# Performance work log

Hardware: AMD Instinct MI355X
Metric: run time of the kernel (lower is better)

Reference implementation:

```python
import jax, jax.numpy as jnp
import numpy as np

B, L, D_IN, D_OUT, K = 2, 4096, 256, 256, 16


def setup_inputs() -> dict:
    key = jax.random.key(0)
    k_u, k_ev, k_ew, k_m = jax.random.split(key, 4)
    u = jax.random.normal(k_u, (B, L, D_IN), dtype=jnp.float32)
    eigenvectors = jax.random.normal(k_ev, (K, L), dtype=jnp.float32)
    # original takes loaded eigenvalues ** 0.25; emulate positive spectrum then 0.25 power
    eigenvalues = jax.random.uniform(k_ew, (K,), dtype=jnp.float32, minval=1e-3, maxval=1.0) ** 0.25
    # xavier_uniform_ for M of shape (k, d_in, d_out): bound = sqrt(6/(d_in+d_out))
    bound = float(np.sqrt(6.0 / (D_IN + D_OUT)))
    M = jax.random.uniform(k_m, (K, D_IN, D_OUT), dtype=jnp.float32, minval=-bound, maxval=bound)
    return {"u": u, "eigenvectors": eigenvectors, "eigenvalues": eigenvalues, "M": M}


def reference(u, eigenvectors, eigenvalues, M):
    # u: (B, L, D); eigenvectors: (k, L); eigenvalues: (k,); M: (k, D_in, D_out)
    Lseq = u.shape[1]
    ev_fft = jnp.fft.rfft(eigenvectors, axis=-1)          # (k, F) complex
    u_fft = jnp.fft.rfft(jnp.swapaxes(u, 1, 2), axis=-1)  # (B, D, F)
    p_fft = u_fft[:, None, :, :] * ev_fft[None, :, None, :]  # (B, k, D, F)
    conv = jnp.fft.irfft(p_fft, n=Lseq, axis=-1)          # (B, k, D, L)
    return jnp.einsum('bkdl,k,kdp->blp', conv, eigenvalues, M)
```

## Files before the change

### kernel.cpp

```cpp
#include <hip/hip_runtime.h>


typedef unsigned int uint;
using u16x8 = __attribute__((ext_vector_type(8))) unsigned short;
using s16x8 = __attribute__((ext_vector_type(8))) short;
using f32x4 = __attribute__((ext_vector_type(4))) float;

__device__ __forceinline__ unsigned short f2bf(float f) {
  uint u = __float_as_uint(f);
  uint r = (u + 0x7FFF + ((u >> 16) & 1)) >> 16;
  return (unsigned short)r;
}
__device__ __forceinline__ float bf2f(unsigned short h) {
  return __uint_as_float(((uint)h) << 16);
}

template <int NT>
__device__ __forceinline__ void fft4096(float2* __restrict__ a,
                                        float2* __restrict__ b,
                                        const float2* __restrict__ tw, int tid) {
  float2* src = a;
  float2* dst = b;
#pragma unroll
  for (int s = 0; s < 12; s += 2) {
    const int m = 1 << s;
#pragma unroll
    for (int it = 0; it < 1024 / NT; ++it) {
      int idx = tid + it * NT;
      int i   = idx & (m - 1);
      int jm  = idx - i;
      float2 A0 = src[idx];
      float2 B0 = src[idx + 1024];
      float2 C0 = src[idx + 2048];
      float2 D0 = src[idx + 3072];
      float2 w1 = tw[jm];
      float2 w2 = make_float2(w1.x * w1.x - w1.y * w1.y, 2.f * w1.x * w1.y);
      float2 w3 = make_float2(w2.x * w1.x - w2.y * w1.y, w2.x * w1.y + w2.y * w1.x);
      float acx = A0.x + C0.x, acy = A0.y + C0.y;
      float amx = A0.x - C0.x, amy = A0.y - C0.y;
      float bdx = B0.x + D0.x, bdy = B0.y + D0.y;
      float bmx = B0.x - D0.x, bmy = B0.y - D0.y;
      float2 y0 = make_float2(acx + bdx, acy + bdy);
      float2 t2 = make_float2(acx - bdx, acy - bdy);
      float2 t1 = make_float2(amx + bmy, amy - bmx);
      float2 t3 = make_float2(amx - bmy, amy + bmx);
      int base = idx + 3 * jm;
      dst[base]         = y0;
      dst[base + m]     = make_float2(w1.x * t1.x - w1.y * t1.y, w1.x * t1.y + w1.y * t1.x);
      dst[base + 2 * m] = make_float2(w2.x * t2.x - w2.y * t2.y, w2.x * t2.y + w2.y * t2.x);
      dst[base + 3 * m] = make_float2(w3.x * t3.x - w3.y * t3.y, w3.x * t3.y + w3.y * t3.x);
    }
    __syncthreads();
    float2* t = src; src = dst; dst = t;
  }
}

template <int NT>
__device__ __forceinline__ void build_tw(float2* tw, int tid) {
  for (int t = tid; t < 1024; t += NT) {
    float ang = -(float)t * (6.283185307179586f / 4096.0f);
    float s, c;
    sincosf(ang, &s, &c);
    tw[t] = make_float2(c, s);
  }
}

__global__ __launch_bounds__(256) void tr_M(const float* __restrict__ M,
                                            unsigned short* __restrict__ Mt) {
  __shared__ float t[64][65];
  const int k = blockIdx.z, d0 = blockIdx.x * 64, p0 = blockIdx.y * 64;
  const int r = threadIdx.x >> 2, c0 = (threadIdx.x & 3) * 16;
  const float* src = M + ((size_t)k * 256 + d0) * 256 + p0;
#pragma unroll
  for (int j = 0; j < 4; ++j) {
    float4 v = *(const float4*)(src + (size_t)r * 256 + c0 + j * 4);
    t[r][c0 + j * 4 + 0] = v.x;
    t[r][c0 + j * 4 + 1] = v.y;
    t[r][c0 + j * 4 + 2] = v.z;
    t[r][c0 + j * 4 + 3] = v.w;
  }
  __syncthreads();
  u16x8 o0, o1;
#pragma unroll
  for (int j = 0; j < 8; ++j) o0[j] = f2bf(t[c0 + j][r]);
#pragma unroll
  for (int j = 0; j < 8; ++j) o1[j] = f2bf(t[c0 + 8 + j][r]);
  unsigned short* dst = Mt + ((size_t)k * 256 + p0 + r) * 256 + d0 + c0;
  *(u16x8*)dst = o0;
  *(u16x8*)(dst + 8) = o1;
}

__global__ __launch_bounds__(1024) void fft_fwd(const float* __restrict__ u,
                                                const float* __restrict__ ev,
                                                const float* __restrict__ lam,
                                                unsigned short* __restrict__ Ut,
                                                float* __restrict__ Hbuf) {
  __shared__ float2 A[4096];
  __shared__ float2 Bb[4096];
  __shared__ float2 tw[1024];
  const int tid = threadIdx.x;
  const int bid = blockIdx.x;
  build_tw<1024>(tw, tid);

  if (bid < 256) {
    const int plane = bid >> 7, pair = bid & 127;
    const int d0 = pair * 2;
    const float* ub = u + (size_t)plane * 4096 * 256 + d0;
#pragma unroll
    for (int i = 0; i < 4; ++i) {
      int l = tid + i * 1024;
      A[l] = *(const float2*)(ub + (size_t)l * 256);
    }
    __syncthreads();
    fft4096<1024>(A, Bb, tw, tid);
    unsigned short* Up = Ut + (size_t)plane * 4096 * 256 + d0;
#pragma unroll
    for (int i = 0; i < 2; ++i) {
      int f = tid + i * 1024;
      float u0x, u0y, u1x, u1y;
      if (f == 0) {
        float2 X0 = A[0], Xn = A[2048];
        u0x = X0.x; u1x = X0.y;
        u0y = Xn.x; u1y = Xn.y;
      } else {
        float2 Xa = A[f], Xb = A[4096 - f];
        u0x = 0.5f * (Xa.x + Xb.x);
        u0y = 0.5f * (Xa.y - Xb.y);
        u1x = 0.5f * (Xa.y + Xb.y);
        u1y = 0.5f * (Xb.x - Xa.x);
      }
      ushort2 re = make_ushort2(f2bf(u0x), f2bf(u1x));
      ushort2 im = make_ushort2(f2bf(u0y), f2bf(u1y));
      *(ushort2*)(Up + (size_t)f * 256)          = re;
      *(ushort2*)(Up + (size_t)(2048 + f) * 256) = im;
    }
  } else {
    const int k = bid - 256;
    const float* eb = ev + (size_t)k * 4096;
#pragma unroll
    for (int i = 0; i < 4; ++i) {
      int l = tid + i * 1024;
      A[l] = make_float2(eb[l], 0.0f);
    }
    __syncthreads();
    fft4096<1024>(A, Bb, tw, tid);
    const float sc = lam[k] * (1.0f / 4096.0f);
    float* Hp = Hbuf + (size_t)k * 4096;
#pragma unroll
    for (int i = 0; i < 2; ++i) {
      int f = tid + i * 1024;
      float2 X = A[f];
      Hp[f] = sc * X.x;
      Hp[2048 + f] = (f == 0) ? sc * A[2048].x : sc * X.y;
    }
  }
}

__global__ __launch_bounds__(256) void gemm_spec(const unsigned short* __restrict__ Ut,
                                                 const unsigned short* __restrict__ Mt,
                                                 const float* __restrict__ Hbuf,
                                                 float* __restrict__ Chat) {
  __shared__ unsigned short Us[128 * 256];
  __shared__ unsigned short Ms[64 * 256];
  const int p0    = blockIdx.x * 64;
  const int fb    = blockIdx.y * 64;
  const int plane = blockIdx.z;
  const int tid  = threadIdx.x;
  const int lane = tid & 63;
  const int wave = tid >> 6;

  const unsigned short* Up = Ut + (size_t)plane * 4096 * 256;
#pragma unroll
  for (int it = 0; it < 16; ++it) {
    int cl = tid + it * 256;
    int r = cl >> 5, c = cl & 31;
    int f2 = (r < 64) ? (fb + r) : (2048 + fb + (r - 64));
    u16x8 v = *(const u16x8*)(Up + (size_t)f2 * 256 + c * 8);
    *(u16x8*)(&Us[r * 256 + ((c ^ (r & 7)) * 8)]) = v;
  }

  u16x8 mreg[8];
#pragma unroll
  for (int it = 0; it < 8; ++it) {
    int cl = tid + it * 256;
    int r = cl >> 5, c = cl & 31;
    mreg[it] = *(const u16x8*)(Mt + (size_t)(p0 + r) * 256 + c * 8);
  }

  f32x4 cre[4], cim[4];
#pragma unroll
  for (int m = 0; m < 4; ++m) {
    cre[m] = (f32x4){0.f, 0.f, 0.f, 0.f};
    cim[m] = (f32x4){0.f, 0.f, 0.f, 0.f};
  }

  const int bin = fb + wave * 16 + (lane & 15);
  const int rb_re = wave * 16 + (lane & 15);
  const int rb_im = 64 + rb_re;

  for (int k = 0; k < 16; ++k) {
    if (k > 0) __syncthreads();
#pragma unroll
    for (int it = 0; it < 8; ++it) {
      int cl = tid + it * 256;
      int r = cl >> 5, c = cl & 31;
      *(u16x8*)(&Ms[r * 256 + ((c ^ (r & 7)) * 8)]) = mreg[it];
    }
    if (k < 15) {
      const unsigned short* Mk = Mt + (size_t)(k + 1) * 65536;
#pragma unroll
      for (int it = 0; it < 8; ++it) {
        int cl = tid + it * 256;
        int r = cl >> 5, c = cl & 31;
        mreg[it] = *(const u16x8*)(Mk + (size_t)(p0 + r) * 256 + c * 8);
      }
    }
    __syncthreads();

    f32x4 are[4], aim[4];
#pragma unroll
    for (int m = 0; m < 4; ++m) {
      are[m] = (f32x4){0.f, 0.f, 0.f, 0.f};
      aim[m] = (f32x4){0.f, 0.f, 0.f, 0.f};
    }
#pragma unroll
    for (int kk = 0; kk < 8; ++kk) {
      const int kc = kk * 4 + (lane >> 4);
      s16x8 bre = *(const s16x8*)(&Us[rb_re * 256 + ((kc ^ (rb_re & 7)) * 8)]);
      s16x8 bim = *(const s16x8*)(&Us[rb_im * 256 + ((kc ^ (rb_im & 7)) * 8)]);
#pragma unroll
      for (int m = 0; m < 4; ++m) {
        int row = m * 16 + (lane & 15);
        s16x8 af = *(const s16x8*)(&Ms[row * 256 + ((kc ^ (row & 7)) * 8)]);
        are[m] = __builtin_amdgcn_mfma_f32_16x16x32_bf16(af, bre, are[m], 0, 0, 0);
        aim[m] = __builtin_amdgcn_mfma_f32_16x16x32_bf16(af, bim, aim[m], 0, 0, 0);
      }
    }
    float hre = Hbuf[(size_t)k * 4096 + bin];
    float hs  = Hbuf[(size_t)k * 4096 + 2048 + bin];
    bool sp = (bin == 0);
    float him = sp ? 0.0f : hs;
    float hA  = sp ? hs : hre;
#pragma unroll
    for (int m = 0; m < 4; ++m)
#pragma unroll
      for (int i = 0; i < 4; ++i) {
        cre[m][i] += hre * are[m][i] - him * aim[m][i];
        cim[m][i] += hA * aim[m][i] + him * are[m][i];
      }
  }

  float* Cp = Chat + ((size_t)plane * 256 + p0) * 4096;
#pragma unroll
  for (int m = 0; m < 4; ++m)
#pragma unroll
    for (int i = 0; i < 4; ++i) {
      int pl = m * 16 + (lane >> 4) * 4 + i;
      Cp[(size_t)pl * 4096 + bin]        = cre[m][i];
      Cp[(size_t)pl * 4096 + 2048 + bin] = cim[m][i];
    }
}

__global__ __launch_bounds__(1024) void ifft_store(const float* __restrict__ Chat,
                                                   float* __restrict__ out) {
  __shared__ float2 A[4096];
  __shared__ float2 Bb[4096];
  __shared__ float2 tw[1024];
  const int tid = threadIdx.x;
  const int p0 = blockIdx.x * 2;
  const int plane = blockIdx.y;
  const float* C0 = Chat + ((size_t)plane * 256 + p0) * 4096;
  const float* C1 = C0 + 4096;
  build_tw<1024>(tw, tid);

  if (tid == 0) {
    A[0]    = make_float2(C0[0], -C1[0]);
    A[2048] = make_float2(C0[2048], -C1[2048]);
  } else {
    int f = tid;
    float cr0 = C0[f], ci0 = C0[2048 + f];
    float cr1 = C1[f], ci1 = C1[2048 + f];
    A[f]        = make_float2(cr0 - ci1, -(ci0 + cr1));
    A[4096 - f] = make_float2(cr0 + ci1, ci0 - cr1);
  }
  {
    int f = tid + 1024;
    float cr0 = C0[f], ci0 = C0[2048 + f];
    float cr1 = C1[f], ci1 = C1[2048 + f];
    A[f]        = make_float2(cr0 - ci1, -(ci0 + cr1));
    A[4096 - f] = make_float2(cr0 + ci1, ci0 - cr1);
  }
  __syncthreads();
  fft4096<1024>(A, Bb, tw, tid);

  float* ob = out + (size_t)plane * 4096 * 256 + p0;
#pragma unroll
  for (int i = 0; i < 4; ++i) {
    int l = tid + i * 1024;
    float2 g = A[l];
    *(float2*)(ob + (size_t)l * 256) = make_float2(g.x, -g.y);
  }
}

extern "C" void kernel_launch(void* const* d_in, const int* in_sizes, int n_in,
                              void* d_out, int out_size, void* d_ws,
                              size_t ws_size, hipStream_t stream) {
  const float* u   = (const float*)d_in[0];
  const float* ev  = (const float*)d_in[1];
  const float* lam = (const float*)d_in[2];
  const float* M   = (const float*)d_in[3];
  float* out = (float*)d_out;

  char* ws = (char*)d_ws;
  float* Hbuf        = (float*)ws;
  unsigned short* Mt = (unsigned short*)(ws + (256 << 10));
  unsigned short* Ut = (unsigned short*)(ws + (256 << 10) + (2 << 20));
  float* Chat        = (float*)(ws + (256 << 10) + (6 << 20));

  tr_M<<<dim3(4, 4, 16), 256, 0, stream>>>(M, Mt);
  fft_fwd<<<272, 1024, 0, stream>>>(u, ev, lam, Ut, Hbuf);
  gemm_spec<<<dim3(4, 32, 2), 256, 0, stream>>>(Ut, Mt, Hbuf, Chat);
  ifft_store<<<dim3(128, 2), 1024, 0, stream>>>(Chat, out);
}
```

Measured before the change: 138.4 us.

## Add transpose kernels for coalesced FFT I/O and split-K GEMM with XCD mapping

Adds separate transpose kernels so the forward FFT reads contiguous bf16 rows and the inverse FFT writes contiguous rows, replacing strided column gathers and scatters with coalesced accesses. The spectral GEMM now runs 512 threads, with two halves each covering 8 of the 16 eigen-components, then sums the halves through shared memory. It also stages H in LDS and remaps blocks across XCDs for locality. In exchange it adds two kernel launches, extra workspace round trips, and a bf16 rounding of u before the FFT, which lowers input precision.

```diff
diff --git a/kernel.cpp b/kernel.cpp
--- a/kernel.cpp
+++ b/kernel.cpp
@@ -90,7 +90,32 @@
   *(u16x8*)(dst + 8) = o1;
 }
 
-__global__ __launch_bounds__(1024) void fft_fwd(const float* __restrict__ u,
+__global__ __launch_bounds__(256) void tr_u(const float* __restrict__ u,
+                                            unsigned short* __restrict__ ubT) {
+  __shared__ float t[64][65];
+  const int l0 = blockIdx.x * 64, d0 = blockIdx.y * 64, plane = blockIdx.z;
+  const int r = threadIdx.x >> 2, c0 = (threadIdx.x & 3) * 16;
+  const float* src = u + ((size_t)plane * 4096 + l0) * 256 + d0;
+#pragma unroll
+  for (int j = 0; j < 4; ++j) {
+    float4 v = *(const float4*)(src + (size_t)r * 256 + c0 + j * 4);
+    t[r][c0 + j * 4 + 0] = v.x;
+    t[r][c0 + j * 4 + 1] = v.y;
+    t[r][c0 + j * 4 + 2] = v.z;
+    t[r][c0 + j * 4 + 3] = v.w;
+  }
+  __syncthreads();
+  u16x8 o0, o1;
+#pragma unroll
+  for (int j = 0; j < 8; ++j) o0[j] = f2bf(t[c0 + j][r]);
+#pragma unroll
+  for (int j = 0; j < 8; ++j) o1[j] = f2bf(t[c0 + 8 + j][r]);
+  unsigned short* dst = ubT + ((size_t)plane * 256 + d0 + r) * 4096 + l0 + c0;
+  *(u16x8*)dst = o0;
+  *(u16x8*)(dst + 8) = o1;
+}
+
+__global__ __launch_bounds__(1024) void fft_fwd(const unsigned short* __restrict__ ubT,
                                                 const float* __restrict__ ev,
                                                 const float* __restrict__ lam,
                                                 unsigned short* __restrict__ Ut,
@@ -103,14 +128,19 @@
   build_tw<1024>(tw, tid);
 
   if (bid < 256) {
-    const int plane = bid >> 7, pair = bid & 127;
+    const int plane = bid >> 7;
+    const int jj = bid & 127;
+    const int pair = (jj & 7) * 16 + (jj >> 3);
     const int d0 = pair * 2;
-    const float* ub = u + (size_t)plane * 4096 * 256 + d0;
-#pragma unroll
-    for (int i = 0; i < 4; ++i) {
-      int l = tid + i * 1024;
-      A[l] = *(const float2*)(ub + (size_t)l * 256);
-    }
+    const unsigned short* r0 = ubT + ((size_t)plane * 256 + d0) * 4096;
+    const unsigned short* r1 = r0 + 4096;
+    const int l0 = tid * 4;
+    ushort4 a4 = *(const ushort4*)(r0 + l0);
+    ushort4 b4 = *(const ushort4*)(r1 + l0);
+    A[l0 + 0] = make_float2(bf2f(a4.x), bf2f(b4.x));
+    A[l0 + 1] = make_float2(bf2f(a4.y), bf2f(b4.y));
+    A[l0 + 2] = make_float2(bf2f(a4.z), bf2f(b4.z));
+    A[l0 + 3] = make_float2(bf2f(a4.w), bf2f(b4.w));
     __syncthreads();
     fft4096<1024>(A, Bb, tw, tid);
     unsigned short* Up = Ut + (size_t)plane * 4096 * 256 + d0;
@@ -156,35 +186,50 @@
   }
 }
 
-__global__ __launch_bounds__(256) void gemm_spec(const unsigned short* __restrict__ Ut,
+__global__ __launch_bounds__(512) void gemm_spec(const unsigned short* __restrict__ Ut,
                                                  const unsigned short* __restrict__ Mt,
                                                  const float* __restrict__ Hbuf,
                                                  float* __restrict__ Chat) {
   __shared__ unsigned short Us[128 * 256];
-  __shared__ unsigned short Ms[64 * 256];
-  const int p0    = blockIdx.x * 64;
-  const int fb    = blockIdx.y * 64;
-  const int plane = blockIdx.z;
+  __shared__ unsigned short Ms[2][64 * 256];
+  __shared__ float Hlds[16 * 128];
+  const int gi  = blockIdx.x;
+  const int xcd = gi & 7;
+  const int gj  = gi >> 3;
+  const int fb    = (xcd * 4 + (gj & 3)) * 64;
+  const int p0    = ((gj >> 2) & 3) * 64;
+  const int plane = gj >> 4;
+
   const int tid  = threadIdx.x;
   const int lane = tid & 63;
   const int wave = tid >> 6;
+  const int half = wave >> 2;
+  const int w4   = wave & 3;
+  const int th   = tid & 255;
 
   const unsigned short* Up = Ut + (size_t)plane * 4096 * 256;
 #pragma unroll
-  for (int it = 0; it < 16; ++it) {
-    int cl = tid + it * 256;
+  for (int it = 0; it < 8; ++it) {
+    int cl = tid + it * 512;
     int r = cl >> 5, c = cl & 31;
     int f2 = (r < 64) ? (fb + r) : (2048 + fb + (r - 64));
     u16x8 v = *(const u16x8*)(Up + (size_t)f2 * 256 + c * 8);
     *(u16x8*)(&Us[r * 256 + ((c ^ (r & 7)) * 8)]) = v;
   }
-
+#pragma unroll
+  for (int it = 0; it < 4; ++it) {
+    int i2 = tid + it * 512;
+    int k = i2 >> 7, rem = i2 & 127;
+    Hlds[i2] = Hbuf[(size_t)k * 4096 + (rem >> 6) * 2048 + fb + (rem & 63)];
+  }
+
+  const unsigned short* Mbase = Mt + (size_t)half * 8 * 65536;
   u16x8 mreg[8];
 #pragma unroll
   for (int it = 0; it < 8; ++it) {
-    int cl = tid + it * 256;
+    int cl = th + it * 256;
     int r = cl >> 5, c = cl & 31;
-    mreg[it] = *(const u16x8*)(Mt + (size_t)(p0 + r) * 256 + c * 8);
+    mreg[it] = *(const u16x8*)(Mbase + (size_t)(p0 + r) * 256 + c * 8);
   }
 
   f32x4 cre[4], cim[4];
@@ -194,23 +239,24 @@
     cim[m] = (f32x4){0.f, 0.f, 0.f, 0.f};
   }
 
-  const int bin = fb + wave * 16 + (lane & 15);
-  const int rb_re = wave * 16 + (lane & 15);
-  const int rb_im = 64 + rb_re;
-
-  for (int k = 0; k < 16; ++k) {
-    if (k > 0) __syncthreads();
+  const int binoff = w4 * 16 + (lane & 15);
+  const int bin = fb + binoff;
+  const int rb_re = binoff;
+  const int rb_im = 64 + binoff;
+
+  for (int kh = 0; kh < 8; ++kh) {
+    if (kh > 0) __syncthreads();
 #pragma unroll
     for (int it = 0; it < 8; ++it) {
-      int cl = tid + it * 256;
+      int cl = th + it * 256;
       int r = cl >> 5, c = cl & 31;
-      *(u16x8*)(&Ms[r * 256 + ((c ^ (r & 7)) * 8)]) = mreg[it];
-    }
-    if (k < 15) {
-      const unsigned short* Mk = Mt + (size_t)(k + 1) * 65536;
+      *(u16x8*)(&Ms[half][r * 256 + ((c ^ (r & 7)) * 8)]) = mreg[it];
+    }
+    if (kh < 7) {
+      const unsigned short* Mk = Mbase + (size_t)(kh + 1) * 65536;
 #pragma unroll
       for (int it = 0; it < 8; ++it) {
-        int cl = tid + it * 256;
+        int cl = th + it * 256;
         int r = cl >> 5, c = cl & 31;
         mreg[it] = *(const u16x8*)(Mk + (size_t)(p0 + r) * 256 + c * 8);
       }
@@ -231,13 +277,14 @@
 #pragma unroll
       for (int m = 0; m < 4; ++m) {
         int row = m * 16 + (lane & 15);
-        s16x8 af = *(const s16x8*)(&Ms[row * 256 + ((kc ^ (row & 7)) * 8)]);
+        s16x8 af = *(const s16x8*)(&Ms[half][row * 256 + ((kc ^ (row & 7)) * 8)]);
         are[m] = __builtin_amdgcn_mfma_f32_16x16x32_bf16(af, bre, are[m], 0, 0, 0);
         aim[m] = __builtin_amdgcn_mfma_f32_16x16x32_bf16(af, bim, aim[m], 0, 0, 0);
       }
     }
-    float hre = Hbuf[(size_t)k * 4096 + bin];
-    float hs  = Hbuf[(size_t)k * 4096 + 2048 + bin];
+    const int k = kh + 8 * half;
+    float hre = Hlds[k * 128 + binoff];
+    float hs  = Hlds[k * 128 + 64 + binoff];
     bool sp = (bin == 0);
     float him = sp ? 0.0f : hs;
     float hA  = sp ? hs : hre;
@@ -250,19 +297,38 @@
       }
   }
 
-  float* Cp = Chat + ((size_t)plane * 256 + p0) * 4096;
+  __syncthreads();
+  float* Red = (float*)Us;
 #pragma unroll
   for (int m = 0; m < 4; ++m)
 #pragma unroll
     for (int i = 0; i < 4; ++i) {
-      int pl = m * 16 + (lane >> 4) * 4 + i;
-      Cp[(size_t)pl * 4096 + bin]        = cre[m][i];
-      Cp[(size_t)pl * 4096 + 2048 + bin] = cim[m][i];
-    }
+      Red[(m * 4 + i) * 512 + tid]        = cre[m][i];
+      Red[(16 + m * 4 + i) * 512 + tid]   = cim[m][i];
+    }
+  __syncthreads();
+  if (tid < 256) {
+#pragma unroll
+    for (int m = 0; m < 4; ++m)
+#pragma unroll
+      for (int i = 0; i < 4; ++i) {
+        cre[m][i] += Red[(m * 4 + i) * 512 + tid + 256];
+        cim[m][i] += Red[(16 + m * 4 + i) * 512 + tid + 256];
+      }
+    float* Cp = Chat + ((size_t)plane * 256 + p0) * 4096;
+#pragma unroll
+    for (int m = 0; m < 4; ++m)
+#pragma unroll
+      for (int i = 0; i < 4; ++i) {
+        int pl = m * 16 + (lane >> 4) * 4 + i;
+        Cp[(size_t)pl * 4096 + bin]        = cre[m][i];
+        Cp[(size_t)pl * 4096 + 2048 + bin] = cim[m][i];
+      }
+  }
 }
 
 __global__ __launch_bounds__(1024) void ifft_store(const float* __restrict__ Chat,
-                                                   float* __restrict__ out) {
+                                                   float* __restrict__ ytmp) {
   __shared__ float2 A[4096];
   __shared__ float2 Bb[4096];
   __shared__ float2 tw[1024];
@@ -293,12 +359,41 @@
   __syncthreads();
   fft4096<1024>(A, Bb, tw, tid);
 
-  float* ob = out + (size_t)plane * 4096 * 256 + p0;
+  float* y0 = ytmp + ((size_t)plane * 256 + p0) * 4096;
+  float* y1 = y0 + 4096;
 #pragma unroll
   for (int i = 0; i < 4; ++i) {
     int l = tid + i * 1024;
     float2 g = A[l];
-    *(float2*)(ob + (size_t)l * 256) = make_float2(g.x, -g.y);
+    y0[l] = g.x;
+    y1[l] = -g.y;
+  }
+}
+
+__global__ __launch_bounds__(256) void tr_out(const float* __restrict__ ytmp,
+                                              float* __restrict__ out) {
+  __shared__ float t[64][65];
+  const int l0 = blockIdx.x * 64, p0 = blockIdx.y * 64, plane = blockIdx.z;
+  const int r = threadIdx.x >> 2, c0 = (threadIdx.x & 3) * 16;
+  const float* src = ytmp + ((size_t)plane * 256 + p0 + r) * 4096 + l0;
+#pragma unroll
+  for (int j = 0; j < 4; ++j) {
+    float4 v = *(const float4*)(src + c0 + j * 4);
+    t[r][c0 + j * 4 + 0] = v.x;
+    t[r][c0 + j * 4 + 1] = v.y;
+    t[r][c0 + j * 4 + 2] = v.z;
+    t[r][c0 + j * 4 + 3] = v.w;
+  }
+  __syncthreads();
+  float* dst = out + ((size_t)plane * 4096 + l0 + r) * 256 + p0 + c0;
+#pragma unroll
+  for (int q = 0; q < 4; ++q) {
+    float4 o;
+    o.x = t[c0 + q * 4 + 0][r];
+    o.y = t[c0 + q * 4 + 1][r];
+    o.z = t[c0 + q * 4 + 2][r];
+    o.w = t[c0 + q * 4 + 3][r];
+    *(float4*)(dst + q * 4) = o;
   }
 }
 
@@ -312,13 +407,17 @@
   float* out = (float*)d_out;
 
   char* ws = (char*)d_ws;
-  float* Hbuf        = (float*)ws;
-  unsigned short* Mt = (unsigned short*)(ws + (256 << 10));
-  unsigned short* Ut = (unsigned short*)(ws + (256 << 10) + (2 << 20));
-  float* Chat        = (float*)(ws + (256 << 10) + (6 << 20));
+  float* Hbuf         = (float*)ws;
+  unsigned short* Mt  = (unsigned short*)(ws + (256 << 10));
+  unsigned short* ubT = (unsigned short*)(ws + (256 << 10) + (2 << 20));
+  unsigned short* Ut  = (unsigned short*)(ws + (256 << 10) + (6 << 20));
+  float* Chat         = (float*)(ws + (256 << 10) + (10 << 20));
+  float* ytmp         = (float*)(ws + (256 << 10) + (18 << 20));
 
   tr_M<<<dim3(4, 4, 16), 256, 0, stream>>>(M, Mt);
-  fft_fwd<<<272, 1024, 0, stream>>>(u, ev, lam, Ut, Hbuf);
-  gemm_spec<<<dim3(4, 32, 2), 256, 0, stream>>>(Ut, Mt, Hbuf, Chat);
-  ifft_store<<<dim3(128, 2), 1024, 0, stream>>>(Chat, out);
-}
+  tr_u<<<dim3(64, 4, 2), 256, 0, stream>>>(u, ubT);
+  fft_fwd<<<272, 1024, 0, stream>>>(ubT, ev, lam, Ut, Hbuf);
+  gemm_spec<<<256, 512, 0, stream>>>(Ut, Mt, Hbuf, Chat);
+  ifft_store<<<dim3(128, 2), 1024, 0, stream>>>(Chat, ytmp);
+  tr_out<<<dim3(64, 4, 2), 256, 0, stream>>>(ytmp, out);
+}
```

New measurement: 120.7 us. 1.15x faster.
